# Kernel optimization log

Measured on AMD Instinct MI355X. Metric: run time of the kernel, lower is better.

The kernel has to match this reference:

```python
import jax, jax.numpy as jnp
import numpy as np

T_TEST, B, F, H, N_OUT = 8192, 8, 100, 512, 1


def setup_inputs() -> dict:
    key = jax.random.key(0)
    ks = jax.random.split(key, 7)
    s = 0.05  # keep generated-weight magnitudes in a realistic hypernetwork range
    return {
        "x_test": jax.random.normal(ks[0], (T_TEST, B, F), dtype=jnp.float32),
        "w1": jax.random.normal(ks[1], (B, F, H), dtype=jnp.float32) * s,
        "b1": jax.random.normal(ks[2], (B, H), dtype=jnp.float32) * s,
        "w2": jax.random.normal(ks[3], (B, H, H), dtype=jnp.float32) * s,
        "b2": jax.random.normal(ks[4], (B, H), dtype=jnp.float32) * s,
        "w3": jax.random.normal(ks[5], (B, H, N_OUT), dtype=jnp.float32) * s,
        "b3": jax.random.normal(ks[6], (B, N_OUT), dtype=jnp.float32) * s,
    }


def reference(x_test, w1, b1, w2, b2, w3, b3):
    # MotherNet.nn_forward with predicted_activation='relu',
    # weight_embedding_rank=None, low_rank_last=False.
    # Original torch: h = (x.unsqueeze(-1) * w.unsqueeze(0)).sum(2) + b
    # == per-dataset batched GEMM over the B axis.
    x = jnp.nan_to_num(x_test)                    # [T, B, F]
    h = jnp.einsum('tbf,bfh->tbh', x, w1) + b1    # [T, B, H]
    h = jax.nn.relu(h)
    h = jnp.einsum('tbf,bfh->tbh', h, w2) + b2    # [T, B, H]
    h = jax.nn.relu(h)
    h = jnp.einsum('tbf,bfh->tbh', h, w3) + b3    # [T, B, 1]
    return h
```

## Files before the change

### kernel.cpp

```cpp
#include <hip/hip_runtime.h>

#define T_TEST 8192
#define BB 8
#define FF 100
#define HH 512

typedef __bf16 bf16x8 __attribute__((ext_vector_type(8)));
typedef float f32x16 __attribute__((ext_vector_type(16)));
typedef unsigned short u16;
typedef unsigned int u32;

__device__ __forceinline__ u16 f2bf(float f) {
    u32 u = __float_as_uint(f);
    u += 0x7fffu + ((u >> 16) & 1);
    return (u16)(u >> 16);
}

__device__ __forceinline__ float nan2num(float v) {
    u32 u = __float_as_uint(v);
    if ((u & 0x7f800000u) == 0x7f800000u) {
        v = (u & 0x007fffffu) ? 0.f : ((u >> 31) ? -3.3895314e38f : 3.3895314e38f);
    }
    return v;
}

__global__ void prep_w(const float* __restrict__ w1, const float* __restrict__ w2,
                       u16* __restrict__ w1f, u16* __restrict__ w2f) {
    int bid = blockIdx.x;
    if (bid < 256) {
        int t = bid * 256 + threadIdx.x;
        int lane = t & 63;
        int n32 = (t >> 6) & 15;
        int ks = (t >> 10) & 7;
        int b = t >> 13;
        int n = n32 * 32 + (lane & 31);
        int kb = ks * 16 + (lane >> 5) * 8;
        u32 p[4];
#pragma unroll
        for (int jp = 0; jp < 4; ++jp) {
            int k0 = kb + jp * 2;
            float v0 = (k0 < FF)     ? w1[(b * FF + k0) * HH + n]     : 0.f;
            float v1 = (k0 + 1 < FF) ? w1[(b * FF + k0 + 1) * HH + n] : 0.f;
            p[jp] = (u32)f2bf(v0) | ((u32)f2bf(v1) << 16);
        }
        uint4 o = {p[0], p[1], p[2], p[3]};
        *(uint4*)(w1f + (size_t)t * 8) = o;
    } else {
        int t = (bid - 256) * 256 + threadIdx.x;
        int lane = t & 63;
        int n32 = (t >> 6) & 15;
        int ks = (t >> 10) & 31;
        int b = t >> 15;
        int n = n32 * 32 + (lane & 31);
        int kb = ks * 16 + (lane >> 5) * 8;
        u32 p[4];
#pragma unroll
        for (int jp = 0; jp < 4; ++jp) {
            int k0 = kb + jp * 2;
            float v0 = w2[(b * HH + k0) * HH + n];
            float v1 = w2[(b * HH + k0 + 1) * HH + n];
            p[jp] = (u32)f2bf(v0) | ((u32)f2bf(v1) << 16);
        }
        uint4 o = {p[0], p[1], p[2], p[3]};
        *(uint4*)(w2f + (size_t)t * 8) = o;
    }
}

__device__ __forceinline__ int x_idx(int row, int k) {
    int g = k >> 3;
    int gp = g ^ (row & 15);
    return row * 128 + gp * 8 + (k & 7);
}
__device__ __forceinline__ int h1_idx(int row, int col) {
    int g = col >> 3;
    int gp = (g & ~15) | ((g ^ row) & 15);
    return row * 512 + gp * 8 + (col & 7);
}

__global__ __launch_bounds__(512, 4) void fused_mlp(
    const float* __restrict__ x, const u16* __restrict__ w1f,
    const float* __restrict__ b1, const u16* __restrict__ w2f,
    const float* __restrict__ b2, const float* __restrict__ w3,
    const float* __restrict__ b3, float* __restrict__ out) {
    __shared__ __align__(16) u16 h1_lds[64 * 512];
    __shared__ __align__(16) u16 x_lds[64 * 128];

    const int tid = threadIdx.x;
    const int b = blockIdx.x;
    const int m0 = blockIdx.y * 64;
    const int lane = tid & 63;
    const int w = tid >> 6;
    const int l31 = lane & 31, lh = lane >> 5;
    const int n32b = w * 2;

    const bf16x8* W1 = (const bf16x8*)w1f + (size_t)b * (8 * 16 * 64);
    const bf16x8* W2 = (const bf16x8*)w2f + (size_t)b * (32 * 16 * 64);

    bf16x8 bb[2][2];
    bb[0][0] = W1[(0 * 16 + n32b + 0) * 64 + lane];
    bb[0][1] = W1[(0 * 16 + n32b + 1) * 64 + lane];
    bb[1][0] = W1[(1 * 16 + n32b + 0) * 64 + lane];
    bb[1][1] = W1[(1 * 16 + n32b + 1) * 64 + lane];

    {
        int row = tid >> 3, sub = tid & 7;
        const float* xr = x + ((size_t)(m0 + row) * BB + b) * FF;
        float4 v0 = *(const float4*)(xr + sub * 4);
        float4 v1 = *(const float4*)(xr + 32 + sub * 4);
        float4 v2 = *(const float4*)(xr + 64 + sub * 4);
        auto xw = [&](int k, float4 v) {
            ushort4 h;
            h.x = f2bf(nan2num(v.x));
            h.y = f2bf(nan2num(v.y));
            h.z = f2bf(nan2num(v.z));
            h.w = f2bf(nan2num(v.w));
            *(ushort4*)(&x_lds[x_idx(row, k)]) = h;
        };
        xw(sub * 4, v0);
        xw(32 + sub * 4, v1);
        xw(64 + sub * 4, v2);
        if (sub == 0) {
            float4 v3 = *(const float4*)(xr + 96);
            xw(96, v3);
            ushort4 z = {0, 0, 0, 0};
            *(ushort4*)(&x_lds[x_idx(row, 100)]) = z;
        } else if (sub <= 3) {
            int4 z = {0, 0, 0, 0};
            *(int4*)(&x_lds[x_idx(row, 96 + sub * 8)]) = z;
        }
    }
    __syncthreads();

    f32x16 acc1[2][2] = {};
#pragma unroll
    for (int ks = 0; ks < 8; ++ks) {
        bf16x8 a0 = *(const bf16x8*)(&x_lds[x_idx(l31,      (2 * ks + lh) * 8)]);
        bf16x8 a1 = *(const bf16x8*)(&x_lds[x_idx(32 + l31, (2 * ks + lh) * 8)]);
        acc1[0][0] = __builtin_amdgcn_mfma_f32_32x32x16_bf16(a0, bb[ks & 1][0], acc1[0][0], 0, 0, 0);
        acc1[0][1] = __builtin_amdgcn_mfma_f32_32x32x16_bf16(a0, bb[ks & 1][1], acc1[0][1], 0, 0, 0);
        acc1[1][0] = __builtin_amdgcn_mfma_f32_32x32x16_bf16(a1, bb[ks & 1][0], acc1[1][0], 0, 0, 0);
        acc1[1][1] = __builtin_amdgcn_mfma_f32_32x32x16_bf16(a1, bb[ks & 1][1], acc1[1][1], 0, 0, 0);
        if (ks < 6) {
            bb[ks & 1][0] = W1[((ks + 2) * 16 + n32b + 0) * 64 + lane];
            bb[ks & 1][1] = W1[((ks + 2) * 16 + n32b + 1) * 64 + lane];
        }
    }

    bb[0][0] = W2[(0 * 16 + n32b + 0) * 64 + lane];
    bb[0][1] = W2[(0 * 16 + n32b + 1) * 64 + lane];
    bb[1][0] = W2[(1 * 16 + n32b + 0) * 64 + lane];
    bb[1][1] = W2[(1 * 16 + n32b + 1) * 64 + lane];

    {
        u32* h32 = (u32*)h1_lds;
        const float* b1g = b1 + b * HH;
#pragma unroll
        for (int ni = 0; ni < 2; ++ni) {
            int n = (n32b + ni) * 32 + l31;
            float b1v = b1g[n];
            int ncol = n & ~1;
#pragma unroll
            for (int mi = 0; mi < 2; ++mi)
#pragma unroll
                for (int qd = 0; qd < 4; ++qd) {
                    u32 own01 = (u32)f2bf(fmaxf(acc1[mi][ni][qd * 4 + 0] + b1v, 0.f)) |
                                ((u32)f2bf(fmaxf(acc1[mi][ni][qd * 4 + 1] + b1v, 0.f)) << 16);
                    u32 own23 = (u32)f2bf(fmaxf(acc1[mi][ni][qd * 4 + 2] + b1v, 0.f)) |
                                ((u32)f2bf(fmaxf(acc1[mi][ni][qd * 4 + 3] + b1v, 0.f)) << 16);
                    u32 oth01 = __shfl_xor(own01, 1, 64);
                    u32 oth23 = __shfl_xor(own23, 1, 64);
                    int row0 = mi * 32 + qd * 8 + lh * 4;
                    if (!(lane & 1)) {
                        u32 d0 = (own01 & 0xffffu) | (oth01 << 16);
                        u32 d1 = (own01 >> 16) | (oth01 & 0xffff0000u);
                        h32[h1_idx(row0, ncol) >> 1] = d0;
                        h32[h1_idx(row0 + 1, ncol) >> 1] = d1;
                    } else {
                        u32 d2 = (oth23 & 0xffffu) | (own23 << 16);
                        u32 d3 = (oth23 >> 16) | (own23 & 0xffff0000u);
                        h32[h1_idx(row0 + 2, ncol) >> 1] = d2;
                        h32[h1_idx(row0 + 3, ncol) >> 1] = d3;
                    }
                }
        }
    }
    __syncthreads();

    f32x16 acc2[2][2] = {};
#pragma unroll
    for (int ks = 0; ks < 32; ++ks) {
        bf16x8 a0 = *(const bf16x8*)(&h1_lds[h1_idx(l31,      (2 * ks + lh) * 8)]);
        bf16x8 a1 = *(const bf16x8*)(&h1_lds[h1_idx(32 + l31, (2 * ks + lh) * 8)]);
        acc2[0][0] = __builtin_amdgcn_mfma_f32_32x32x16_bf16(a0, bb[ks & 1][0], acc2[0][0], 0, 0, 0);
        acc2[0][1] = __builtin_amdgcn_mfma_f32_32x32x16_bf16(a0, bb[ks & 1][1], acc2[0][1], 0, 0, 0);
        acc2[1][0] = __builtin_amdgcn_mfma_f32_32x32x16_bf16(a1, bb[ks & 1][0], acc2[1][0], 0, 0, 0);
        acc2[1][1] = __builtin_amdgcn_mfma_f32_32x32x16_bf16(a1, bb[ks & 1][1], acc2[1][1], 0, 0, 0);
        if (ks < 30) {
            bb[ks & 1][0] = W2[((ks + 2) * 16 + n32b + 0) * 64 + lane];
            bb[ks & 1][1] = W2[((ks + 2) * 16 + n32b + 1) * 64 + lane];
        }
    }

    const float* b2g = b2 + b * HH;
    const float* w3g = w3 + b * HH;
    float b2v0 = b2g[(n32b + 0) * 32 + l31], w3v0 = w3g[(n32b + 0) * 32 + l31];
    float b2v1 = b2g[(n32b + 1) * 32 + l31], w3v1 = w3g[(n32b + 1) * 32 + l31];
    float* part = (float*)x_lds;
#pragma unroll
    for (int mi = 0; mi < 2; ++mi)
#pragma unroll
        for (int r = 0; r < 16; ++r) {
            float v = fmaxf(acc2[mi][0][r] + b2v0, 0.f) * w3v0 +
                      fmaxf(acc2[mi][1][r] + b2v1, 0.f) * w3v1;
            v += __shfl_xor(v, 1, 64);
            v += __shfl_xor(v, 2, 64);
            v += __shfl_xor(v, 4, 64);
            v += __shfl_xor(v, 8, 64);
            v += __shfl_xor(v, 16, 64);
            if (l31 == 0)
                part[w * 64 + mi * 32 + (r & 3) + 8 * (r >> 2) + 4 * lh] = v;
        }
    __syncthreads();
    if (tid < 64) {
        float s = b3[b];
#pragma unroll
        for (int ww = 0; ww < 8; ++ww) s += part[ww * 64 + tid];
        out[(size_t)(m0 + tid) * BB + b] = s;
    }
}

extern "C" void kernel_launch(void* const* d_in, const int* in_sizes, int n_in,
                              void* d_out, int out_size, void* d_ws, size_t ws_size,
                              hipStream_t stream) {
    const float* x  = (const float*)d_in[0];
    const float* w1 = (const float*)d_in[1];
    const float* b1 = (const float*)d_in[2];
    const float* w2 = (const float*)d_in[3];
    const float* b2 = (const float*)d_in[4];
    const float* w3 = (const float*)d_in[5];
    const float* b3 = (const float*)d_in[6];
    float* out = (float*)d_out;

    u16* w1f = (u16*)d_ws;
    u16* w2f = w1f + (size_t)BB * 8192 * 8;

    prep_w<<<1280, 256, 0, stream>>>(w1, w2, w1f, w2f);

    fused_mlp<<<dim3(BB, T_TEST / 64), 512, 0, stream>>>(
        x, w1f, b1, w2f, b2, w3, b3, out);
}
```

Baseline: 137.3 us.

## Triple-buffer A/B fragments and stagger per-wave K start to avoid LDS conflicts

Both MFMA loops now prefetch the LDS A-fragments along with the global B-fragments two steps ahead, using a three-slot register ring. Each wave starts its K iteration at a different offset (wave id for layer 1, wave*4 for layer 2), so waves hit different LDS banks and weight cache lines at the same moment. The aim is to hide LDS and global load latency behind MFMAs. The extra fragment registers raise VGPR pressure under launch_bounds(512,4), which could cause spilling or lower occupancy.

```diff
diff --git a/kernel.cpp b/kernel.cpp
--- a/kernel.cpp
+++ b/kernel.cpp
@@ -31,10 +31,9 @@
         int t = bid * 256 + threadIdx.x;
         int lane = t & 63;
         int n32 = (t >> 6) & 15;
-        int ks = (t >> 10) & 7;
         int b = t >> 13;
         int n = n32 * 32 + (lane & 31);
-        int kb = ks * 16 + (lane >> 5) * 8;
+        int kb = ((t >> 10) & 7) * 16 + (lane >> 5) * 8;
         u32 p[4];
 #pragma unroll
         for (int jp = 0; jp < 4; ++jp) {
@@ -49,10 +48,9 @@
         int t = (bid - 256) * 256 + threadIdx.x;
         int lane = t & 63;
         int n32 = (t >> 6) & 15;
-        int ks = (t >> 10) & 31;
         int b = t >> 15;
         int n = n32 * 32 + (lane & 31);
-        int kb = ks * 16 + (lane >> 5) * 8;
+        int kb = ((t >> 10) & 31) * 16 + (lane >> 5) * 8;
         u32 p[4];
 #pragma unroll
         for (int jp = 0; jp < 4; ++jp) {
@@ -92,15 +90,21 @@
     const int w = tid >> 6;
     const int l31 = lane & 31, lh = lane >> 5;
     const int n32b = w * 2;
+    const int r1 = w;
+    const int r2 = (w * 4) & 31;
 
     const bf16x8* W1 = (const bf16x8*)w1f + (size_t)b * (8 * 16 * 64);
     const bf16x8* W2 = (const bf16x8*)w2f + (size_t)b * (32 * 16 * 64);
 
-    bf16x8 bb[2][2];
-    bb[0][0] = W1[(0 * 16 + n32b + 0) * 64 + lane];
-    bb[0][1] = W1[(0 * 16 + n32b + 1) * 64 + lane];
-    bb[1][0] = W1[(1 * 16 + n32b + 0) * 64 + lane];
-    bb[1][1] = W1[(1 * 16 + n32b + 1) * 64 + lane];
+    bf16x8 aa[3][2], bb[3][2];
+
+    {
+        int k0 = r1, k1 = (r1 + 1) & 7;
+        bb[0][0] = W1[(k0 * 16 + n32b + 0) * 64 + lane];
+        bb[0][1] = W1[(k0 * 16 + n32b + 1) * 64 + lane];
+        bb[1][0] = W1[(k1 * 16 + n32b + 0) * 64 + lane];
+        bb[1][1] = W1[(k1 * 16 + n32b + 1) * 64 + lane];
+    }
 
     {
         int row = tid >> 3, sub = tid & 7;
@@ -132,24 +136,37 @@
     __syncthreads();
 
     f32x16 acc1[2][2] = {};
+    {
+        int k0 = r1, k1 = (r1 + 1) & 7;
+        aa[0][0] = *(const bf16x8*)(&x_lds[x_idx(l31,      (2 * k0 + lh) * 8)]);
+        aa[0][1] = *(const bf16x8*)(&x_lds[x_idx(32 + l31, (2 * k0 + lh) * 8)]);
+        aa[1][0] = *(const bf16x8*)(&x_lds[x_idx(l31,      (2 * k1 + lh) * 8)]);
+        aa[1][1] = *(const bf16x8*)(&x_lds[x_idx(32 + l31, (2 * k1 + lh) * 8)]);
+    }
 #pragma unroll
     for (int ks = 0; ks < 8; ++ks) {
-        bf16x8 a0 = *(const bf16x8*)(&x_lds[x_idx(l31,      (2 * ks + lh) * 8)]);
-        bf16x8 a1 = *(const bf16x8*)(&x_lds[x_idx(32 + l31, (2 * ks + lh) * 8)]);
-        acc1[0][0] = __builtin_amdgcn_mfma_f32_32x32x16_bf16(a0, bb[ks & 1][0], acc1[0][0], 0, 0, 0);
-        acc1[0][1] = __builtin_amdgcn_mfma_f32_32x32x16_bf16(a0, bb[ks & 1][1], acc1[0][1], 0, 0, 0);
-        acc1[1][0] = __builtin_amdgcn_mfma_f32_32x32x16_bf16(a1, bb[ks & 1][0], acc1[1][0], 0, 0, 0);
-        acc1[1][1] = __builtin_amdgcn_mfma_f32_32x32x16_bf16(a1, bb[ks & 1][1], acc1[1][1], 0, 0, 0);
+        const int p = ks % 3;
         if (ks < 6) {
-            bb[ks & 1][0] = W1[((ks + 2) * 16 + n32b + 0) * 64 + lane];
-            bb[ks & 1][1] = W1[((ks + 2) * 16 + n32b + 1) * 64 + lane];
-        }
-    }
-
-    bb[0][0] = W2[(0 * 16 + n32b + 0) * 64 + lane];
-    bb[0][1] = W2[(0 * 16 + n32b + 1) * 64 + lane];
-    bb[1][0] = W2[(1 * 16 + n32b + 0) * 64 + lane];
-    bb[1][1] = W2[(1 * 16 + n32b + 1) * 64 + lane];
+            const int f = (ks + 2) % 3;
+            int ksp = (ks + 2 + r1) & 7;
+            aa[f][0] = *(const bf16x8*)(&x_lds[x_idx(l31,      (2 * ksp + lh) * 8)]);
+            aa[f][1] = *(const bf16x8*)(&x_lds[x_idx(32 + l31, (2 * ksp + lh) * 8)]);
+            bb[f][0] = W1[(ksp * 16 + n32b + 0) * 64 + lane];
+            bb[f][1] = W1[(ksp * 16 + n32b + 1) * 64 + lane];
+        }
+        acc1[0][0] = __builtin_amdgcn_mfma_f32_32x32x16_bf16(aa[p][0], bb[p][0], acc1[0][0], 0, 0, 0);
+        acc1[0][1] = __builtin_amdgcn_mfma_f32_32x32x16_bf16(aa[p][0], bb[p][1], acc1[0][1], 0, 0, 0);
+        acc1[1][0] = __builtin_amdgcn_mfma_f32_32x32x16_bf16(aa[p][1], bb[p][0], acc1[1][0], 0, 0, 0);
+        acc1[1][1] = __builtin_amdgcn_mfma_f32_32x32x16_bf16(aa[p][1], bb[p][1], acc1[1][1], 0, 0, 0);
+    }
+
+    {
+        int k0 = r2, k1 = (r2 + 1) & 31;
+        bb[0][0] = W2[(k0 * 16 + n32b + 0) * 64 + lane];
+        bb[0][1] = W2[(k0 * 16 + n32b + 1) * 64 + lane];
+        bb[1][0] = W2[(k1 * 16 + n32b + 0) * 64 + lane];
+        bb[1][1] = W2[(k1 * 16 + n32b + 1) * 64 + lane];
+    }
 
     {
         u32* h32 = (u32*)h1_lds;
@@ -187,18 +204,28 @@
     __syncthreads();
 
     f32x16 acc2[2][2] = {};
+    {
+        int k0 = r2, k1 = (r2 + 1) & 31;
+        aa[0][0] = *(const bf16x8*)(&h1_lds[h1_idx(l31,      (2 * k0 + lh) * 8)]);
+        aa[0][1] = *(const bf16x8*)(&h1_lds[h1_idx(32 + l31, (2 * k0 + lh) * 8)]);
+        aa[1][0] = *(const bf16x8*)(&h1_lds[h1_idx(l31,      (2 * k1 + lh) * 8)]);
+        aa[1][1] = *(const bf16x8*)(&h1_lds[h1_idx(32 + l31, (2 * k1 + lh) * 8)]);
+    }
 #pragma unroll
     for (int ks = 0; ks < 32; ++ks) {
-        bf16x8 a0 = *(const bf16x8*)(&h1_lds[h1_idx(l31,      (2 * ks + lh) * 8)]);
-        bf16x8 a1 = *(const bf16x8*)(&h1_lds[h1_idx(32 + l31, (2 * ks + lh) * 8)]);
-        acc2[0][0] = __builtin_amdgcn_mfma_f32_32x32x16_bf16(a0, bb[ks & 1][0], acc2[0][0], 0, 0, 0);
-        acc2[0][1] = __builtin_amdgcn_mfma_f32_32x32x16_bf16(a0, bb[ks & 1][1], acc2[0][1], 0, 0, 0);
-        acc2[1][0] = __builtin_amdgcn_mfma_f32_32x32x16_bf16(a1, bb[ks & 1][0], acc2[1][0], 0, 0, 0);
-        acc2[1][1] = __builtin_amdgcn_mfma_f32_32x32x16_bf16(a1, bb[ks & 1][1], acc2[1][1], 0, 0, 0);
+        const int p = ks % 3;
         if (ks < 30) {
-            bb[ks & 1][0] = W2[((ks + 2) * 16 + n32b + 0) * 64 + lane];
-            bb[ks & 1][1] = W2[((ks + 2) * 16 + n32b + 1) * 64 + lane];
-        }
+            const int f = (ks + 2) % 3;
+            int ksp = (ks + 2 + r2) & 31;
+            aa[f][0] = *(const bf16x8*)(&h1_lds[h1_idx(l31,      (2 * ksp + lh) * 8)]);
+            aa[f][1] = *(const bf16x8*)(&h1_lds[h1_idx(32 + l31, (2 * ksp + lh) * 8)]);
+            bb[f][0] = W2[(ksp * 16 + n32b + 0) * 64 + lane];
+            bb[f][1] = W2[(ksp * 16 + n32b + 1) * 64 + lane];
+        }
+        acc2[0][0] = __builtin_amdgcn_mfma_f32_32x32x16_bf16(aa[p][0], bb[p][0], acc2[0][0], 0, 0, 0);
+        acc2[0][1] = __builtin_amdgcn_mfma_f32_32x32x16_bf16(aa[p][0], bb[p][1], acc2[0][1], 0, 0, 0);
+        acc2[1][0] = __builtin_amdgcn_mfma_f32_32x32x16_bf16(aa[p][1], bb[p][0], acc2[1][0], 0, 0, 0);
+        acc2[1][1] = __builtin_amdgcn_mfma_f32_32x32x16_bf16(aa[p][1], bb[p][1], acc2[1][1], 0, 0, 0);
     }
 
     const float* b2g = b2 + b * HH;
```

Result: slower. 140.4 us (+2.3%).

## Use 4 waves per block with 64x128 wave tiles and 3-stage register prefetch

Applied to the files above, without the earlier changes.

Halves the block to 256 threads so each wave computes a 64x128 output tile (4 N-subtiles instead of 2), which doubles the MFMA work per A-fragment load from LDS. Both A (LDS) and B (global) fragments are now prefetched through a 3-deep rotating register buffer, and each wave starts its K loop at a staggered offset to spread out LDS bank and memory accesses. The cost is a larger register footprint (accumulators go from 4 to 8 f32x16 tiles) and fewer waves per block, which can lower occupancy and latency hiding.

```diff
diff --git a/kernel.cpp b/kernel.cpp
--- a/kernel.cpp
+++ b/kernel.cpp
@@ -31,10 +31,9 @@
         int t = bid * 256 + threadIdx.x;
         int lane = t & 63;
         int n32 = (t >> 6) & 15;
-        int ks = (t >> 10) & 7;
         int b = t >> 13;
         int n = n32 * 32 + (lane & 31);
-        int kb = ks * 16 + (lane >> 5) * 8;
+        int kb = ((t >> 10) & 7) * 16 + (lane >> 5) * 8;
         u32 p[4];
 #pragma unroll
         for (int jp = 0; jp < 4; ++jp) {
@@ -49,10 +48,9 @@
         int t = (bid - 256) * 256 + threadIdx.x;
         int lane = t & 63;
         int n32 = (t >> 6) & 15;
-        int ks = (t >> 10) & 31;
         int b = t >> 15;
         int n = n32 * 32 + (lane & 31);
-        int kb = ks * 16 + (lane >> 5) * 8;
+        int kb = ((t >> 10) & 31) * 16 + (lane >> 5) * 8;
         u32 p[4];
 #pragma unroll
         for (int jp = 0; jp < 4; ++jp) {
@@ -77,7 +75,7 @@
     return row * 512 + gp * 8 + (col & 7);
 }
 
-__global__ __launch_bounds__(512, 4) void fused_mlp(
+__global__ __launch_bounds__(256, 2) void fused_mlp(
     const float* __restrict__ x, const u16* __restrict__ w1f,
     const float* __restrict__ b1, const u16* __restrict__ w2f,
     const float* __restrict__ b2, const float* __restrict__ w3,
@@ -89,73 +87,92 @@
     const int b = blockIdx.x;
     const int m0 = blockIdx.y * 64;
     const int lane = tid & 63;
-    const int w = tid >> 6;
+    const int ws = __builtin_amdgcn_readfirstlane(tid >> 6);
     const int l31 = lane & 31, lh = lane >> 5;
-    const int n32b = w * 2;
+    const int n32b = ws * 4;
+    const int r1 = (ws * 2) & 7;
+    const int r2 = (ws * 8) & 31;
 
     const bf16x8* W1 = (const bf16x8*)w1f + (size_t)b * (8 * 16 * 64);
     const bf16x8* W2 = (const bf16x8*)w2f + (size_t)b * (32 * 16 * 64);
 
-    bf16x8 bb[2][2];
-    bb[0][0] = W1[(0 * 16 + n32b + 0) * 64 + lane];
-    bb[0][1] = W1[(0 * 16 + n32b + 1) * 64 + lane];
-    bb[1][0] = W1[(1 * 16 + n32b + 0) * 64 + lane];
-    bb[1][1] = W1[(1 * 16 + n32b + 1) * 64 + lane];
+    bf16x8 pa[3][2], pb[3][4];
+
+#pragma unroll
+    for (int s = 0; s < 2; ++s) {
+        int k = (r1 + s) & 7;
+#pragma unroll
+        for (int ni = 0; ni < 4; ++ni)
+            pb[s][ni] = W1[(k * 16 + n32b + ni) * 64 + lane];
+    }
 
     {
-        int row = tid >> 3, sub = tid & 7;
+        int row = tid >> 2, sub = tid & 3;
         const float* xr = x + ((size_t)(m0 + row) * BB + b) * FF;
-        float4 v0 = *(const float4*)(xr + sub * 4);
-        float4 v1 = *(const float4*)(xr + 32 + sub * 4);
-        float4 v2 = *(const float4*)(xr + 64 + sub * 4);
-        auto xw = [&](int k, float4 v) {
-            ushort4 h;
-            h.x = f2bf(nan2num(v.x));
-            h.y = f2bf(nan2num(v.y));
-            h.z = f2bf(nan2num(v.z));
-            h.w = f2bf(nan2num(v.w));
-            *(ushort4*)(&x_lds[x_idx(row, k)]) = h;
-        };
-        xw(sub * 4, v0);
-        xw(32 + sub * 4, v1);
-        xw(64 + sub * 4, v2);
+#pragma unroll
+        for (int j = 0; j < 7; ++j) {
+            int k = sub * 4 + j * 16;
+            if (k < FF) {
+                float4 v = *(const float4*)(xr + k);
+                ushort4 h;
+                h.x = f2bf(nan2num(v.x));
+                h.y = f2bf(nan2num(v.y));
+                h.z = f2bf(nan2num(v.z));
+                h.w = f2bf(nan2num(v.w));
+                *(ushort4*)(&x_lds[x_idx(row, k)]) = h;
+            }
+        }
         if (sub == 0) {
-            float4 v3 = *(const float4*)(xr + 96);
-            xw(96, v3);
             ushort4 z = {0, 0, 0, 0};
             *(ushort4*)(&x_lds[x_idx(row, 100)]) = z;
-        } else if (sub <= 3) {
+        } else {
             int4 z = {0, 0, 0, 0};
             *(int4*)(&x_lds[x_idx(row, 96 + sub * 8)]) = z;
         }
     }
     __syncthreads();
 
-    f32x16 acc1[2][2] = {};
+    f32x16 acc1[2][4] = {};
+#pragma unroll
+    for (int s = 0; s < 2; ++s) {
+        int k = (r1 + s) & 7;
+#pragma unroll
+        for (int mi = 0; mi < 2; ++mi)
+            pa[s][mi] = *(const bf16x8*)(&x_lds[x_idx(mi * 32 + l31, (2 * k + lh) * 8)]);
+    }
 #pragma unroll
     for (int ks = 0; ks < 8; ++ks) {
-        bf16x8 a0 = *(const bf16x8*)(&x_lds[x_idx(l31,      (2 * ks + lh) * 8)]);
-        bf16x8 a1 = *(const bf16x8*)(&x_lds[x_idx(32 + l31, (2 * ks + lh) * 8)]);
-        acc1[0][0] = __builtin_amdgcn_mfma_f32_32x32x16_bf16(a0, bb[ks & 1][0], acc1[0][0], 0, 0, 0);
-        acc1[0][1] = __builtin_amdgcn_mfma_f32_32x32x16_bf16(a0, bb[ks & 1][1], acc1[0][1], 0, 0, 0);
-        acc1[1][0] = __builtin_amdgcn_mfma_f32_32x32x16_bf16(a1, bb[ks & 1][0], acc1[1][0], 0, 0, 0);
-        acc1[1][1] = __builtin_amdgcn_mfma_f32_32x32x16_bf16(a1, bb[ks & 1][1], acc1[1][1], 0, 0, 0);
+        const int p = ks % 3;
         if (ks < 6) {
-            bb[ks & 1][0] = W1[((ks + 2) * 16 + n32b + 0) * 64 + lane];
-            bb[ks & 1][1] = W1[((ks + 2) * 16 + n32b + 1) * 64 + lane];
-        }
-    }
-
-    bb[0][0] = W2[(0 * 16 + n32b + 0) * 64 + lane];
-    bb[0][1] = W2[(0 * 16 + n32b + 1) * 64 + lane];
-    bb[1][0] = W2[(1 * 16 + n32b + 0) * 64 + lane];
-    bb[1][1] = W2[(1 * 16 + n32b + 1) * 64 + lane];
+            const int f = (ks + 2) % 3;
+            int kf = (ks + 2 + r1) & 7;
+#pragma unroll
+            for (int mi = 0; mi < 2; ++mi)
+                pa[f][mi] = *(const bf16x8*)(&x_lds[x_idx(mi * 32 + l31, (2 * kf + lh) * 8)]);
+#pragma unroll
+            for (int ni = 0; ni < 4; ++ni)
+                pb[f][ni] = W1[(kf * 16 + n32b + ni) * 64 + lane];
+        }
+#pragma unroll
+        for (int ni = 0; ni < 4; ++ni) {
+            acc1[0][ni] = __builtin_amdgcn_mfma_f32_32x32x16_bf16(pa[p][0], pb[p][ni], acc1[0][ni], 0, 0, 0);
+            acc1[1][ni] = __builtin_amdgcn_mfma_f32_32x32x16_bf16(pa[p][1], pb[p][ni], acc1[1][ni], 0, 0, 0);
+        }
+    }
+
+#pragma unroll
+    for (int s = 0; s < 2; ++s) {
+        int k = (r2 + s) & 31;
+#pragma unroll
+        for (int ni = 0; ni < 4; ++ni)
+            pb[s][ni] = W2[(k * 16 + n32b + ni) * 64 + lane];
+    }
 
     {
         u32* h32 = (u32*)h1_lds;
         const float* b1g = b1 + b * HH;
 #pragma unroll
-        for (int ni = 0; ni < 2; ++ni) {
+        for (int ni = 0; ni < 4; ++ni) {
             int n = (n32b + ni) * 32 + l31;
             float b1v = b1g[n];
             int ncol = n & ~1;
@@ -186,45 +203,65 @@
     }
     __syncthreads();
 
-    f32x16 acc2[2][2] = {};
+    f32x16 acc2[2][4] = {};
+#pragma unroll
+    for (int s = 0; s < 2; ++s) {
+        int k = (r2 + s) & 31;
+#pragma unroll
+        for (int mi = 0; mi < 2; ++mi)
+            pa[s][mi] = *(const bf16x8*)(&h1_lds[h1_idx(mi * 32 + l31, (2 * k + lh) * 8)]);
+    }
 #pragma unroll
     for (int ks = 0; ks < 32; ++ks) {
-        bf16x8 a0 = *(const bf16x8*)(&h1_lds[h1_idx(l31,      (2 * ks + lh) * 8)]);
-        bf16x8 a1 = *(const bf16x8*)(&h1_lds[h1_idx(32 + l31, (2 * ks + lh) * 8)]);
-        acc2[0][0] = __builtin_amdgcn_mfma_f32_32x32x16_bf16(a0, bb[ks & 1][0], acc2[0][0], 0, 0, 0);
-        acc2[0][1] = __builtin_amdgcn_mfma_f32_32x32x16_bf16(a0, bb[ks & 1][1], acc2[0][1], 0, 0, 0);
-        acc2[1][0] = __builtin_amdgcn_mfma_f32_32x32x16_bf16(a1, bb[ks & 1][0], acc2[1][0], 0, 0, 0);
-        acc2[1][1] = __builtin_amdgcn_mfma_f32_32x32x16_bf16(a1, bb[ks & 1][1], acc2[1][1], 0, 0, 0);
+        const int p = ks % 3;
         if (ks < 30) {
-            bb[ks & 1][0] = W2[((ks + 2) * 16 + n32b + 0) * 64 + lane];
-            bb[ks & 1][1] = W2[((ks + 2) * 16 + n32b + 1) * 64 + lane];
+            const int f = (ks + 2) % 3;
+            int kf = (ks + 2 + r2) & 31;
+#pragma unroll
+            for (int mi = 0; mi < 2; ++mi)
+                pa[f][mi] = *(const bf16x8*)(&h1_lds[h1_idx(mi * 32 + l31, (2 * kf + lh) * 8)]);
+#pragma unroll
+            for (int ni = 0; ni < 4; ++ni)
+                pb[f][ni] = W2[(kf * 16 + n32b + ni) * 64 + lane];
+        }
+#pragma unroll
+        for (int ni = 0; ni < 4; ++ni) {
+            acc2[0][ni] = __builtin_amdgcn_mfma_f32_32x32x16_bf16(pa[p][0], pb[p][ni], acc2[0][ni], 0, 0, 0);
+            acc2[1][ni] = __builtin_amdgcn_mfma_f32_32x32x16_bf16(pa[p][1], pb[p][ni], acc2[1][ni], 0, 0, 0);
         }
     }
 
     const float* b2g = b2 + b * HH;
     const float* w3g = w3 + b * HH;
-    float b2v0 = b2g[(n32b + 0) * 32 + l31], w3v0 = w3g[(n32b + 0) * 32 + l31];
-    float b2v1 = b2g[(n32b + 1) * 32 + l31], w3v1 = w3g[(n32b + 1) * 32 + l31];
+    float b2v[4], w3v[4];
+#pragma unroll
+    for (int ni = 0; ni < 4; ++ni) {
+        int n = (n32b + ni) * 32 + l31;
+        b2v[ni] = b2g[n];
+        w3v[ni] = w3g[n];
+    }
     float* part = (float*)x_lds;
 #pragma unroll
     for (int mi = 0; mi < 2; ++mi)
 #pragma unroll
         for (int r = 0; r < 16; ++r) {
-            float v = fmaxf(acc2[mi][0][r] + b2v0, 0.f) * w3v0 +
-                      fmaxf(acc2[mi][1][r] + b2v1, 0.f) * w3v1;
+            float v = 0.f;
+#pragma unroll
+            for (int ni = 0; ni < 4; ++ni)
+                v += fmaxf(acc2[mi][ni][r] + b2v[ni], 0.f) * w3v[ni];
             v += __shfl_xor(v, 1, 64);
             v += __shfl_xor(v, 2, 64);
             v += __shfl_xor(v, 4, 64);
             v += __shfl_xor(v, 8, 64);
             v += __shfl_xor(v, 16, 64);
             if (l31 == 0)
-                part[w * 64 + mi * 32 + (r & 3) + 8 * (r >> 2) + 4 * lh] = v;
+                part[ws * 64 + mi * 32 + (r & 3) + 8 * (r >> 2) + 4 * lh] = v;
         }
     __syncthreads();
     if (tid < 64) {
         float s = b3[b];
 #pragma unroll
-        for (int ww = 0; ww < 8; ++ww) s += part[ww * 64 + tid];
+        for (int ww = 0; ww < 4; ++ww) s += part[ww * 64 + tid];
         out[(size_t)(m0 + tid) * BB + b] = s;
     }
 }
@@ -246,6 +283,6 @@
 
     prep_w<<<1280, 256, 0, stream>>>(w1, w2, w1f, w2f);
 
-    fused_mlp<<<dim3(BB, T_TEST / 64), 512, 0, stream>>>(
+    fused_mlp<<<dim3(BB, T_TEST / 64), 256, 0, stream>>>(
         x, w1f, b1, w2f, b2, w3, b3, out);
 }
```

Measured after the change: 153.3 us. 1.12x slower.
